# Performance work log

Hardware: AMD Instinct MI355X
Metric: run time of the kernel (lower is better)

## Reference

```python
import jax, jax.numpy as jnp
import numpy as np

B, N, D, F, NRBF, H = 8, 256, 3, 32, 50, 128
EPS = 1e-6

# Levi-Civita tensor [3,3,3]
LC = jnp.array(np.array([[[0, 0, 0], [0, 0, 1], [0, -1, 0]],
                         [[0, 0, -1], [0, 0, 0], [1, 0, 0]],
                         [[0, 1, 0], [-1, 0, 0], [0, 0, 0]]], dtype=np.float32))

# off-diagonal neighbor indices: OFFD[i] = all j != i  -> [N, N-1]
OFFD = np.stack([np.concatenate([np.arange(i), np.arange(i + 1, N)]) for i in range(N)])


def mlp(x, W1, b1, W2, b2):
    return jax.nn.silu(x @ W1 + b1) @ W2 + b2


def rbf_encode(d, mus, gamma):
    # d: [B,N,N-1,1] -> [B,N,N-1,NRBF]
    return jnp.exp(-gamma * (d - mus) ** 2)


def setup_inputs() -> dict:
    key = jax.random.key(0)
    ks = jax.random.split(key, 8)
    p = lambda k, shape: 0.1 * jax.random.normal(k, shape, dtype=jnp.float32)
    IN = NRBF + 2 * F    # 114: rbfs + self feats + 'other' feats
    INF = NRBF + F       # 82: rbfs + softmax feats
    return {
        't': jnp.zeros((1,), jnp.float32),
        'state': jax.random.normal(ks[0], (B, N * D + N * F), dtype=jnp.float32),
        'mus': jnp.linspace(0.0, 5.0, NRBF, dtype=jnp.float32),
        'gamma': jnp.float32(10.0),
        's1_W1': p(ks[1], (IN, H)), 's1_b1': jnp.zeros((H,), jnp.float32),
        's1_W2': p(ks[2], (H, 1)), 's1_b2': jnp.zeros((1,), jnp.float32),
        's2_W1': p(ks[3], (IN, H)), 's2_b1': jnp.zeros((H,), jnp.float32),
        's2_W2': p(ks[4], (H, 1)), 's2_b2': jnp.zeros((1,), jnp.float32),
        'f_W1': p(ks[5], (INF, H)), 'f_b1': jnp.zeros((H,), jnp.float32),
        'f_W2': p(ks[6], (H, F)), 'f_b2': jnp.zeros((F,), jnp.float32),
    }


def reference(t, state, mus, gamma,
              s1_W1, s1_b1, s1_W2, s1_b2,
              s2_W1, s2_b1, s2_W2, s2_b2,
              f_W1, f_b1, f_W2, f_b2):
    x = state[:, :N * D].reshape(B, N, D)
    feats = state[:, N * D:].reshape(B, N, F)

    # distance vectors r[b,i,k] = x[b,i] - x[b, OFFD[i,k]]  -> [B,N,N-1,D]
    r = x[:, :, None, :] - x[:, OFFD, :]
    d = jnp.sqrt(jnp.sum(r ** 2, -1, keepdims=True) + EPS)  # [B,N,N-1,1]

    # NOTE: the torch tile+transpose+diagonal_filter yields other_feats[b,i,k] = feats[b,i]
    # (self features broadcast over neighbors); reproduced faithfully.
    feats_i = jnp.broadcast_to(feats[:, :, None, :], (B, N, N - 1, F))
    other_feats = feats_i

    rbfs = rbf_encode(d, mus, gamma)  # [B,N,N-1,NRBF]
    inp = jnp.concatenate([rbfs, feats_i, other_feats], -1)  # [B,N,N-1,114]

    # exact trace: grad of s1 wrt d contracted with r2d (torch.autograd.grad equivalent)
    def s1_of_d(dd):
        rb = rbf_encode(dd, mus, gamma)
        return mlp(jnp.concatenate([rb, feats_i, other_feats], -1), s1_W1, s1_b1, s1_W2, s1_b2)

    s1, vjp_fn = jax.vjp(s1_of_d, d)  # s1: [B,N,N-1,1]
    r2d = jnp.sum(r ** 2, -1, keepdims=True) / d
    (gd,) = vjp_fn(r2d)
    first_sum = jnp.sum(gd, axis=(1, 2))          # [B,1]
    second_sum = jnp.sum(s1 * D, axis=(1, 2))     # [B,1]
    trace = (first_sum + second_sum) / (N - 1)    # [B,1]

    s2 = mlp(inp, s2_W1, s2_b1, s2_W2, s2_b2)     # [B,N,N-1,1]

    # feature dynamics: cat(rbfs, softmax(other_feats)) -> MLP -> mean over neighbors
    inp_f = jnp.concatenate([rbfs, jax.nn.softmax(other_feats, axis=-1)], -1)
    v_feats = mlp(inp_f, f_W1, f_b1, f_W2, f_b2).mean(axis=2).reshape(B, N * F)

    v_x = (r * s1).mean(axis=2)  # [B,N,D]
    rr = jnp.einsum('ofi,nabf,nai->nabo', LC, r, v_x)  # [B,N,N-1,D]
    v_x = v_x + (rr * s2).mean(axis=2)
    v_x = (v_x - v_x.mean(axis=1, keepdims=True)).reshape(B, N * D)  # remove_mean

    v = jnp.concatenate([v_x, v_feats], axis=-1)  # [B, N*D + N*F]
    return v, trace
```

## Files before the change

kernel.cpp:

```cpp
#include <hip/hip_runtime.h>
#include <math.h>

#define Bn 8
#define Nn 256
#define Fn 32
#define NRBF 50
#define Hn 128
#define NK 255
#define ROW 8960
#define EPSf 1e-6f
#define KP 64
#define L2E 1.44269504f

typedef __attribute__((ext_vector_type(8))) __bf16 b8;
typedef __attribute__((ext_vector_type(4))) float f32x4;

__device__ __forceinline__ float fast_sig(float z) {
    return __builtin_amdgcn_rcpf(1.f + __builtin_amdgcn_exp2f(-z * L2E));
}

__device__ __forceinline__ int aswz(int row, int ch) {
    return row * KP + ((ch ^ (row & 7)) << 3);
}

__global__ __launch_bounds__(256) void prep_kernel(
    const float* __restrict__ s1_W1, const float* __restrict__ s1_b1,
    const float* __restrict__ s2_W1, const float* __restrict__ s2_b1,
    const float* __restrict__ f_W1,  const float* __restrict__ f_b1,
    const float* __restrict__ mus,   const float* __restrict__ state,
    __bf16* __restrict__ Wb,
    float* __restrict__ zb1, float* __restrict__ zb2, float* __restrict__ zb3)
{
    const int tid = threadIdx.x;
    if (blockIdx.x < 128) {
        int idx = blockIdx.x * 256 + tid;
        int g = idx >> 13;
        int h = (idx >> 6) & 127;
        int k = idx & 63;
        float v = 0.f;
        if (k < NRBF) {
            if (g == 0)      v = s1_W1[k * Hn + h];
            else if (g == 1) v = s1_W1[k * Hn + h] * mus[k];
            else if (g == 2) v = s2_W1[k * Hn + h];
            else             v = f_W1[k * Hn + h];
        }
        Wb[idx] = (__bf16)v;
        return;
    }

    const int p = blockIdx.x - 128;
    const int b = p >> 8, i = p & 255;

    __shared__ float ff[Fn], sf[Fn];
    if (tid < Fn) ff[tid] = state[b * ROW + Nn * 3 + i * Fn + tid];
    __syncthreads();
    if (tid < Fn) {
        float mx = -1e30f;
        for (int f = 0; f < Fn; f++) mx = fmaxf(mx, ff[f]);
        sf[tid] = __builtin_amdgcn_exp2f((ff[tid] - mx) * L2E);
    }
    __syncthreads();
    if (tid < Fn) {
        float s = 0.f;
        for (int f = 0; f < Fn; f++) s += sf[f];
        sf[tid] = sf[tid] * __builtin_amdgcn_rcpf(s);
    }
    __syncthreads();

    const int h = tid & 127;
    if (tid < 128) {
        float z1 = s1_b1[h], z2 = s2_b1[h];
        for (int f = 0; f < Fn; f++) {
            float fv = ff[f];
            z1 += fv * (s1_W1[(NRBF + f) * Hn + h] + s1_W1[(NRBF + Fn + f) * Hn + h]);
            z2 += fv * (s2_W1[(NRBF + f) * Hn + h] + s2_W1[(NRBF + Fn + f) * Hn + h]);
        }
        zb1[p * Hn + h] = z1;
        zb2[p * Hn + h] = z2;
    } else {
        float zf = f_b1[h];
        for (int f = 0; f < Fn; f++)
            zf += sf[f] * f_W1[(NRBF + f) * Hn + h];
        zb3[p * Hn + h] = zf;
    }
}

__global__ __launch_bounds__(256, 2) void pair_kernel(
    const float* __restrict__ state,
    const float* __restrict__ mus,   const float* __restrict__ gammap,
    const float* __restrict__ s1_W2, const float* __restrict__ s1_b2,
    const float* __restrict__ s2_W2, const float* __restrict__ s2_b2,
    const float* __restrict__ f_W2,  const float* __restrict__ f_b2,
    const __bf16* __restrict__ Wb,
    const float* __restrict__ zb1, const float* __restrict__ zb2,
    const float* __restrict__ zb3,
    float* __restrict__ vx_pre, float* __restrict__ tr_part,
    float* __restrict__ out)
{
    const int i = blockIdx.x, b = blockIdx.y;
    const int pi = b * Nn + i;
    const int tid  = threadIdx.x;
    const int w    = tid >> 6;
    const int lane = tid & 63;
    const int c    = lane & 15;
    const int q    = lane >> 4;

    __shared__ __attribute__((aligned(16))) __bf16 As[256 * KP];
    __shared__ float xpos[Nn * 3];
    __shared__ float musS[52];
    __shared__ float zf1s[Hn], zf2s[Hn], zffs[Hn];
    __shared__ float sW2a[Hn], sW2b[Hn];
    __shared__ float afsumsh[Hn];
    __shared__ float accum7[8];

    for (int t = tid; t < Nn * 3; t += 256) xpos[t] = state[b * ROW + t];
    if (tid < NRBF) musS[tid] = mus[tid];
    if (tid < Hn) {
        zf1s[tid] = zb1[pi * Hn + tid];
        zf2s[tid] = zb2[pi * Hn + tid];
        zffs[tid] = zb3[pi * Hn + tid];
        sW2a[tid] = s1_W2[tid];
        sW2b[tid] = s2_W2[tid];
        afsumsh[tid] = 0.f;
    }
    if (tid < 8) accum7[tid] = 0.f;
    __syncthreads();

    const float gamma = gammap[0];

    {
        const float valid = (tid < NK) ? 1.f : 0.f;
        const int   kk    = (tid < NK) ? tid : 0;
        const int   j     = kk + (kk >= i ? 1 : 0);
        float rx = (xpos[i * 3 + 0] - xpos[j * 3 + 0]) * valid;
        float ry = (xpos[i * 3 + 1] - xpos[j * 3 + 1]) * valid;
        float rz = (xpos[i * 3 + 2] - xpos[j * 3 + 2]) * valid;
        float ssq = rx * rx + ry * ry + rz * rz;
        float dd  = sqrtf(ssq + EPSf);
        const float ngl = -gamma * L2E;
        #pragma unroll
        for (int ch = 0; ch < 8; ch++) {
            b8 v;
            #pragma unroll
            for (int jj = 0; jj < 8; jj++) {
                int m = ch * 8 + jj;
                float rv = 0.f;
                if (m < NRBF) {
                    float t = dd - musS[m];
                    rv = __builtin_amdgcn_exp2f(ngl * t * t) * valid;
                }
                v[jj] = (__bf16)rv;
            }
            *(b8*)&As[aswz(tid, ch)] = v;
        }
    }
    __syncthreads();

    const int row0 = w * 64;

    float s1p[16], ds1a[16], ds1b[16], s2p[16];
    #pragma unroll
    for (int t = 0; t < 16; t++) { s1p[t] = 0.f; ds1a[t] = 0.f; ds1b[t] = 0.f; s2p[t] = 0.f; }

    {
        b8 a0[4], a1[4];
        #pragma unroll
        for (int mc = 0; mc < 4; mc++) {
            int rrow = row0 + mc * 16 + c;
            a0[mc] = *(const b8*)&As[aswz(rrow, q)];
            a1[mc] = *(const b8*)&As[aswz(rrow, 4 + q)];
        }
        for (int nt = 0; nt < 8; nt++) {
            int h = nt * 16 + c;
            const b8* B0 = (const b8*)&Wb[(0 * Hn + h) * KP];
            const b8* B1 = (const b8*)&Wb[(1 * Hn + h) * KP];
            b8 b00 = B0[q], b01 = B0[4 + q];
            b8 b10 = B1[q], b11 = B1[4 + q];
            float w2  = sW2a[h];
            float zf1 = zf1s[h];
            #pragma unroll
            for (int mc = 0; mc < 4; mc++) {
                f32x4 acc1 = {0.f, 0.f, 0.f, 0.f}, accm = {0.f, 0.f, 0.f, 0.f};
                acc1 = __builtin_amdgcn_mfma_f32_16x16x32_bf16(a0[mc], b00, acc1, 0, 0, 0);
                acc1 = __builtin_amdgcn_mfma_f32_16x16x32_bf16(a1[mc], b01, acc1, 0, 0, 0);
                accm = __builtin_amdgcn_mfma_f32_16x16x32_bf16(a0[mc], b10, accm, 0, 0, 0);
                accm = __builtin_amdgcn_mfma_f32_16x16x32_bf16(a1[mc], b11, accm, 0, 0, 0);
                #pragma unroll
                for (int r = 0; r < 4; r++) {
                    int idx = mc * 4 + r;
                    float zr1 = acc1[r];
                    float z1  = zr1 + zf1;
                    float sig = fast_sig(z1);
                    s1p[idx]  = fmaf(z1 * sig, w2, s1p[idx]);
                    float cc  = w2 * (sig * fmaf(z1, 1.f - sig, 1.f));
                    ds1a[idx] = fmaf(cc, zr1, ds1a[idx]);
                    ds1b[idx] = fmaf(cc, accm[r], ds1b[idx]);
                }
            }
        }
    }

    {
        b8 a0[4], a1[4];
        #pragma unroll
        for (int mc = 0; mc < 4; mc++) {
            int rrow = row0 + mc * 16 + c;
            a0[mc] = *(const b8*)&As[aswz(rrow, q)];
            a1[mc] = *(const b8*)&As[aswz(rrow, 4 + q)];
        }
        for (int nt = 0; nt < 8; nt++) {
            int h = nt * 16 + c;
            const b8* B2 = (const b8*)&Wb[(2 * Hn + h) * KP];
            b8 b20 = B2[q], b21 = B2[4 + q];
            float w2  = sW2b[h];
            float zf2 = zf2s[h];
            #pragma unroll
            for (int mc = 0; mc < 4; mc++) {
                f32x4 acc = {0.f, 0.f, 0.f, 0.f};
                acc = __builtin_amdgcn_mfma_f32_16x16x32_bf16(a0[mc], b20, acc, 0, 0, 0);
                acc = __builtin_amdgcn_mfma_f32_16x16x32_bf16(a1[mc], b21, acc, 0, 0, 0);
                #pragma unroll
                for (int r = 0; r < 4; r++) {
                    int idx = mc * 4 + r;
                    float z2  = acc[r] + zf2;
                    s2p[idx]  = fmaf(z2 * fast_sig(z2), w2, s2p[idx]);
                }
            }
        }
    }

    {
        const float b2_1 = (c == 0) ? s1_b2[0] : 0.f;
        const float b2_2 = (c == 0) ? s2_b2[0] : 0.f;
        const float n2g  = -2.f * gamma;
        const float xi0 = xpos[i * 3 + 0], xi1 = xpos[i * 3 + 1], xi2 = xpos[i * 3 + 2];
        float p0 = 0.f, p1 = 0.f, p2 = 0.f, p3 = 0.f, p4 = 0.f, p5 = 0.f, p6 = 0.f;
        #pragma unroll
        for (int mc = 0; mc < 4; mc++)
            #pragma unroll
            for (int r = 0; r < 4; r++) {
                int idx = mc * 4 + r;
                int row = row0 + mc * 16 + q * 4 + r;
                if (row < NK) {
                    int j = row + (row >= i ? 1 : 0);
                    float rx = xi0 - xpos[j * 3 + 0];
                    float ry = xi1 - xpos[j * 3 + 1];
                    float rz = xi2 - xpos[j * 3 + 2];
                    float ssq = rx * rx + ry * ry + rz * rz;
                    float dd  = sqrtf(ssq + EPSf);
                    float e1  = s1p[idx] + b2_1;
                    float e2  = s2p[idx] + b2_2;
                    float e3  = fmaf(dd, ds1a[idx], -ds1b[idx]);
                    float fr  = n2g * ssq * __builtin_amdgcn_rcpf(dd);
                    p0 = fmaf(rx, e1, p0); p1 = fmaf(ry, e1, p1); p2 = fmaf(rz, e1, p2);
                    p3 = fmaf(rx, e2, p3); p4 = fmaf(ry, e2, p4); p5 = fmaf(rz, e2, p5);
                    p6 = fmaf(fr, e3, fmaf(3.f, e1, p6));
                }
            }
        float ps[7] = {p0, p1, p2, p3, p4, p5, p6};
        #pragma unroll
        for (int off = 1; off < 64; off <<= 1)
            #pragma unroll
            for (int t = 0; t < 7; t++) ps[t] += __shfl_xor(ps[t], off, 64);
        if (lane == 0) {
            #pragma unroll
            for (int t = 0; t < 7; t++) atomicAdd(&accum7[t], ps[t]);
        }
    }

    {
        b8 a0[4], a1[4];
        #pragma unroll
        for (int mc = 0; mc < 4; mc++) {
            int rrow = row0 + mc * 16 + c;
            a0[mc] = *(const b8*)&As[aswz(rrow, q)];
            a1[mc] = *(const b8*)&As[aswz(rrow, 4 + q)];
        }
        for (int nt = 0; nt < 8; nt++) {
            int h = nt * 16 + c;
            const b8* B3 = (const b8*)&Wb[(3 * Hn + h) * KP];
            b8 b30 = B3[q], b31 = B3[4 + q];
            float zff = zffs[h];
            float afp = 0.f;
            #pragma unroll
            for (int mc = 0; mc < 4; mc++) {
                f32x4 acc = {0.f, 0.f, 0.f, 0.f};
                acc = __builtin_amdgcn_mfma_f32_16x16x32_bf16(a0[mc], b30, acc, 0, 0, 0);
                acc = __builtin_amdgcn_mfma_f32_16x16x32_bf16(a1[mc], b31, acc, 0, 0, 0);
                #pragma unroll
                for (int r = 0; r < 4; r++) {
                    int row = row0 + mc * 16 + q * 4 + r;
                    float z  = acc[r] + zff;
                    float av = z * fast_sig(z);
                    afp += (row < NK) ? av : 0.f;
                }
            }
            afp += __shfl_xor(afp, 16, 64);
            afp += __shfl_xor(afp, 32, 64);
            if (lane < 16) atomicAdd(&afsumsh[h], afp);
        }
    }
    __syncthreads();

    if (tid == 0) {
        const float inv = 1.f / 255.f;
        float vx0 = accum7[0] * inv, vx1 = accum7[1] * inv, vx2 = accum7[2] * inv;
        float cx = (accum7[4] * vx2 - accum7[5] * vx1) * inv;
        float cy = (accum7[5] * vx0 - accum7[3] * vx2) * inv;
        float cz = (accum7[3] * vx1 - accum7[4] * vx0) * inv;
        vx_pre[pi * 4 + 0] = vx0 + cx;
        vx_pre[pi * 4 + 1] = vx1 + cy;
        vx_pre[pi * 4 + 2] = vx2 + cz;
        tr_part[pi] = accum7[6];
    }

    if (tid < Fn) {
        float acc = 0.f;
        for (int h = 0; h < Hn; h++) acc = fmaf(afsumsh[h], f_W2[h * Fn + tid], acc);
        out[b * ROW + Nn * 3 + i * Fn + tid] = fmaf(acc, 1.f / 255.f, f_b2[tid]);
    }
}

__global__ __launch_bounds__(256) void finalize_kernel(
    const float* __restrict__ vx_pre, const float* __restrict__ tr_part,
    float* __restrict__ out)
{
    int b = blockIdx.x, tid = threadIdx.x;
    int bi = b * Nn + tid;
    float v0 = vx_pre[bi * 4 + 0];
    float v1 = vx_pre[bi * 4 + 1];
    float v2 = vx_pre[bi * 4 + 2];
    float tr = tr_part[bi];

    __shared__ float red[4][4];
    __shared__ float fin[4];
    float vals[4] = {v0, v1, v2, tr};
    #pragma unroll
    for (int cc = 0; cc < 4; cc++) {
        float v = vals[cc];
        #pragma unroll
        for (int off = 32; off; off >>= 1) v += __shfl_down(v, off, 64);
        if ((tid & 63) == 0) red[tid >> 6][cc] = v;
    }
    __syncthreads();
    if (tid < 4) fin[tid] = red[0][tid] + red[1][tid] + red[2][tid] + red[3][tid];
    __syncthreads();

    out[b * ROW + tid * 3 + 0] = v0 - fin[0] * (1.f / 256.f);
    out[b * ROW + tid * 3 + 1] = v1 - fin[1] * (1.f / 256.f);
    out[b * ROW + tid * 3 + 2] = v2 - fin[2] * (1.f / 256.f);
    if (tid == 0) out[Bn * ROW + b] = fin[3] * (1.f / 255.f);
}

extern "C" void kernel_launch(void* const* d_in, const int* in_sizes, int n_in,
                              void* d_out, int out_size, void* d_ws, size_t ws_size,
                              hipStream_t stream)
{
    const float* state = (const float*)d_in[1];
    const float* mus   = (const float*)d_in[2];
    const float* gam   = (const float*)d_in[3];
    const float* s1_W1 = (const float*)d_in[4];
    const float* s1_b1 = (const float*)d_in[5];
    const float* s1_W2 = (const float*)d_in[6];
    const float* s1_b2 = (const float*)d_in[7];
    const float* s2_W1 = (const float*)d_in[8];
    const float* s2_b1 = (const float*)d_in[9];
    const float* s2_W2 = (const float*)d_in[10];
    const float* s2_b2 = (const float*)d_in[11];
    const float* f_W1  = (const float*)d_in[12];
    const float* f_b1  = (const float*)d_in[13];
    const float* f_W2  = (const float*)d_in[14];
    const float* f_b2  = (const float*)d_in[15];

    char* wsb = (char*)d_ws;
    __bf16* Wb   = (__bf16*)wsb;
    float* zb1   = (float*)(wsb + 65536);
    float* zb2   = zb1 + Bn * Nn * Hn;
    float* zb3   = zb2 + Bn * Nn * Hn;
    float* vx_pre  = zb3 + Bn * Nn * Hn;
    float* tr_part = vx_pre + Bn * Nn * 4;
    float* out   = (float*)d_out;

    prep_kernel<<<128 + Bn * Nn, 256, 0, stream>>>(
        s1_W1, s1_b1, s2_W1, s2_b1, f_W1, f_b1, mus, state, Wb, zb1, zb2, zb3);

    dim3 grid(Nn, Bn);
    pair_kernel<<<grid, 256, 0, stream>>>(state, mus, gam,
        s1_W2, s1_b2, s2_W2, s2_b2, f_W2, f_b2,
        Wb, zb1, zb2, zb3, vx_pre, tr_part, out);

    finalize_kernel<<<Bn, 256, 0, stream>>>(vx_pre, tr_part, out);
}
```

Baseline: 203.0 us.

## Build RBF MFMA operands in registers instead of staging through LDS

New measurement: 207.1 us. 2.0% more time.

```diff
diff --git a/kernel.cpp b/kernel.cpp
--- a/kernel.cpp
+++ b/kernel.cpp
@@ -17,10 +17,6 @@
 
 __device__ __forceinline__ float fast_sig(float z) {
     return __builtin_amdgcn_rcpf(1.f + __builtin_amdgcn_exp2f(-z * L2E));
-}
-
-__device__ __forceinline__ int aswz(int row, int ch) {
-    return row * KP + ((ch ^ (row & 7)) << 3);
 }
 
 __global__ __launch_bounds__(256) void prep_kernel(
@@ -105,7 +101,6 @@
     const int c    = lane & 15;
     const int q    = lane >> 4;
 
-    __shared__ __attribute__((aligned(16))) __bf16 As[256 * KP];
     __shared__ float xpos[Nn * 3];
     __shared__ float musS[52];
     __shared__ float zf1s[Hn], zf2s[Hn], zffs[Hn];
@@ -115,6 +110,7 @@
 
     for (int t = tid; t < Nn * 3; t += 256) xpos[t] = state[b * ROW + t];
     if (tid < NRBF) musS[tid] = mus[tid];
+    if (tid >= NRBF && tid < 52) musS[tid] = 0.f;
     if (tid < Hn) {
         zf1s[tid] = zb1[pi * Hn + tid];
         zf2s[tid] = zb2[pi * Hn + tid];
@@ -127,113 +123,117 @@
     __syncthreads();
 
     const float gamma = gammap[0];
-
-    {
-        const float valid = (tid < NK) ? 1.f : 0.f;
-        const int   kk    = (tid < NK) ? tid : 0;
-        const int   j     = kk + (kk >= i ? 1 : 0);
-        float rx = (xpos[i * 3 + 0] - xpos[j * 3 + 0]) * valid;
-        float ry = (xpos[i * 3 + 1] - xpos[j * 3 + 1]) * valid;
-        float rz = (xpos[i * 3 + 2] - xpos[j * 3 + 2]) * valid;
+    const float ngl   = -gamma * L2E;
+    const int   row0  = w * 64;
+    const float xi0 = xpos[i * 3 + 0], xi1 = xpos[i * 3 + 1], xi2 = xpos[i * 3 + 2];
+
+    b8 a0[4], a1[4];
+    #pragma unroll
+    for (int mc = 0; mc < 4; mc++) {
+        int row = row0 + mc * 16 + c;
+        int kk  = (row < NK) ? row : 0;
+        float valid = (row < NK) ? 1.f : 0.f;
+        int j = kk + (kk >= i ? 1 : 0);
+        float rx = xi0 - xpos[j * 3 + 0];
+        float ry = xi1 - xpos[j * 3 + 1];
+        float rz = xi2 - xpos[j * 3 + 2];
         float ssq = rx * rx + ry * ry + rz * rz;
         float dd  = sqrtf(ssq + EPSf);
-        const float ngl = -gamma * L2E;
-        #pragma unroll
-        for (int ch = 0; ch < 8; ch++) {
-            b8 v;
-            #pragma unroll
-            for (int jj = 0; jj < 8; jj++) {
-                int m = ch * 8 + jj;
-                float rv = 0.f;
-                if (m < NRBF) {
-                    float t = dd - musS[m];
-                    rv = __builtin_amdgcn_exp2f(ngl * t * t) * valid;
-                }
-                v[jj] = (__bf16)rv;
-            }
-            *(b8*)&As[aswz(tid, ch)] = v;
-        }
-    }
-    __syncthreads();
-
-    const int row0 = w * 64;
+        #pragma unroll
+        for (int jj = 0; jj < 8; jj++) {
+            float t = dd - musS[q * 8 + jj];
+            a0[mc][jj] = (__bf16)(__builtin_amdgcn_exp2f(ngl * t * t) * valid);
+        }
+        #pragma unroll
+        for (int jj = 0; jj < 8; jj++) {
+            int k = 32 + q * 8 + jj;
+            float t = dd - musS[(k < NRBF) ? k : 50];
+            float rv = (k < NRBF) ? __builtin_amdgcn_exp2f(ngl * t * t) * valid : 0.f;
+            a1[mc][jj] = (__bf16)rv;
+        }
+    }
 
     float s1p[16], ds1a[16], ds1b[16], s2p[16];
     #pragma unroll
     for (int t = 0; t < 16; t++) { s1p[t] = 0.f; ds1a[t] = 0.f; ds1b[t] = 0.f; s2p[t] = 0.f; }
 
-    {
-        b8 a0[4], a1[4];
+    for (int nt = 0; nt < 8; nt++) {
+        int h = nt * 16 + c;
+        const b8* B0 = (const b8*)&Wb[(0 * Hn + h) * KP];
+        const b8* B1 = (const b8*)&Wb[(1 * Hn + h) * KP];
+        b8 b00 = B0[q], b01 = B0[4 + q];
+        b8 b10 = B1[q], b11 = B1[4 + q];
+        float w2  = sW2a[h];
+        float zf1 = zf1s[h];
         #pragma unroll
         for (int mc = 0; mc < 4; mc++) {
-            int rrow = row0 + mc * 16 + c;
-            a0[mc] = *(const b8*)&As[aswz(rrow, q)];
-            a1[mc] = *(const b8*)&As[aswz(rrow, 4 + q)];
-        }
-        for (int nt = 0; nt < 8; nt++) {
-            int h = nt * 16 + c;
-            const b8* B0 = (const b8*)&Wb[(0 * Hn + h) * KP];
-            const b8* B1 = (const b8*)&Wb[(1 * Hn + h) * KP];
-            b8 b00 = B0[q], b01 = B0[4 + q];
-            b8 b10 = B1[q], b11 = B1[4 + q];
-            float w2  = sW2a[h];
-            float zf1 = zf1s[h];
-            #pragma unroll
-            for (int mc = 0; mc < 4; mc++) {
-                f32x4 acc1 = {0.f, 0.f, 0.f, 0.f}, accm = {0.f, 0.f, 0.f, 0.f};
-                acc1 = __builtin_amdgcn_mfma_f32_16x16x32_bf16(a0[mc], b00, acc1, 0, 0, 0);
-                acc1 = __builtin_amdgcn_mfma_f32_16x16x32_bf16(a1[mc], b01, acc1, 0, 0, 0);
-                accm = __builtin_amdgcn_mfma_f32_16x16x32_bf16(a0[mc], b10, accm, 0, 0, 0);
-                accm = __builtin_amdgcn_mfma_f32_16x16x32_bf16(a1[mc], b11, accm, 0, 0, 0);
-                #pragma unroll
-                for (int r = 0; r < 4; r++) {
-                    int idx = mc * 4 + r;
-                    float zr1 = acc1[r];
-                    float z1  = zr1 + zf1;
-                    float sig = fast_sig(z1);
-                    s1p[idx]  = fmaf(z1 * sig, w2, s1p[idx]);
-                    float cc  = w2 * (sig * fmaf(z1, 1.f - sig, 1.f));
-                    ds1a[idx] = fmaf(cc, zr1, ds1a[idx]);
-                    ds1b[idx] = fmaf(cc, accm[r], ds1b[idx]);
-                }
+            f32x4 acc1 = {0.f, 0.f, 0.f, 0.f}, accm = {0.f, 0.f, 0.f, 0.f};
+            acc1 = __builtin_amdgcn_mfma_f32_16x16x32_bf16(a0[mc], b00, acc1, 0, 0, 0);
+            acc1 = __builtin_amdgcn_mfma_f32_16x16x32_bf16(a1[mc], b01, acc1, 0, 0, 0);
+            accm = __builtin_amdgcn_mfma_f32_16x16x32_bf16(a0[mc], b10, accm, 0, 0, 0);
+            accm = __builtin_amdgcn_mfma_f32_16x16x32_bf16(a1[mc], b11, accm, 0, 0, 0);
+            #pragma unroll
+            for (int r = 0; r < 4; r++) {
+                int idx = mc * 4 + r;
+                float zr1 = acc1[r];
+                float z1  = zr1 + zf1;
+                float sig = fast_sig(z1);
+                s1p[idx]  = fmaf(z1 * sig, w2, s1p[idx]);
+                float cc  = w2 * (sig * fmaf(z1, 1.f - sig, 1.f));
+                ds1a[idx] = fmaf(cc, zr1, ds1a[idx]);
+                ds1b[idx] = fmaf(cc, accm[r], ds1b[idx]);
             }
         }
     }
 
-    {
-        b8 a0[4], a1[4];
+    for (int nt = 0; nt < 8; nt++) {
+        int h = nt * 16 + c;
+        const b8* B2 = (const b8*)&Wb[(2 * Hn + h) * KP];
+        b8 b20 = B2[q], b21 = B2[4 + q];
+        float w2  = sW2b[h];
+        float zf2 = zf2s[h];
         #pragma unroll
         for (int mc = 0; mc < 4; mc++) {
-            int rrow = row0 + mc * 16 + c;
-            a0[mc] = *(const b8*)&As[aswz(rrow, q)];
-            a1[mc] = *(const b8*)&As[aswz(rrow, 4 + q)];
-        }
-        for (int nt = 0; nt < 8; nt++) {
-            int h = nt * 16 + c;
-            const b8* B2 = (const b8*)&Wb[(2 * Hn + h) * KP];
-            b8 b20 = B2[q], b21 = B2[4 + q];
-            float w2  = sW2b[h];
-            float zf2 = zf2s[h];
-            #pragma unroll
-            for (int mc = 0; mc < 4; mc++) {
-                f32x4 acc = {0.f, 0.f, 0.f, 0.f};
-                acc = __builtin_amdgcn_mfma_f32_16x16x32_bf16(a0[mc], b20, acc, 0, 0, 0);
-                acc = __builtin_amdgcn_mfma_f32_16x16x32_bf16(a1[mc], b21, acc, 0, 0, 0);
-                #pragma unroll
-                for (int r = 0; r < 4; r++) {
-                    int idx = mc * 4 + r;
-                    float z2  = acc[r] + zf2;
-                    s2p[idx]  = fmaf(z2 * fast_sig(z2), w2, s2p[idx]);
-                }
+            f32x4 acc = {0.f, 0.f, 0.f, 0.f};
+            acc = __builtin_amdgcn_mfma_f32_16x16x32_bf16(a0[mc], b20, acc, 0, 0, 0);
+            acc = __builtin_amdgcn_mfma_f32_16x16x32_bf16(a1[mc], b21, acc, 0, 0, 0);
+            #pragma unroll
+            for (int r = 0; r < 4; r++) {
+                int idx = mc * 4 + r;
+                float z2  = acc[r] + zf2;
+                s2p[idx]  = fmaf(z2 * fast_sig(z2), w2, s2p[idx]);
             }
         }
+    }
+
+    for (int nt = 0; nt < 8; nt++) {
+        int h = nt * 16 + c;
+        const b8* B3 = (const b8*)&Wb[(3 * Hn + h) * KP];
+        b8 b30 = B3[q], b31 = B3[4 + q];
+        float zff = zffs[h];
+        float afp = 0.f;
+        #pragma unroll
+        for (int mc = 0; mc < 4; mc++) {
+            f32x4 acc = {0.f, 0.f, 0.f, 0.f};
+            acc = __builtin_amdgcn_mfma_f32_16x16x32_bf16(a0[mc], b30, acc, 0, 0, 0);
+            acc = __builtin_amdgcn_mfma_f32_16x16x32_bf16(a1[mc], b31, acc, 0, 0, 0);
+            #pragma unroll
+            for (int r = 0; r < 4; r++) {
+                int row = row0 + mc * 16 + q * 4 + r;
+                float z  = acc[r] + zff;
+                float av = z * fast_sig(z);
+                afp += (row < NK) ? av : 0.f;
+            }
+        }
+        afp += __shfl_xor(afp, 16, 64);
+        afp += __shfl_xor(afp, 32, 64);
+        if (lane < 16) atomicAdd(&afsumsh[h], afp);
     }
 
     {
         const float b2_1 = (c == 0) ? s1_b2[0] : 0.f;
         const float b2_2 = (c == 0) ? s2_b2[0] : 0.f;
         const float n2g  = -2.f * gamma;
-        const float xi0 = xpos[i * 3 + 0], xi1 = xpos[i * 3 + 1], xi2 = xpos[i * 3 + 2];
         float p0 = 0.f, p1 = 0.f, p2 = 0.f, p3 = 0.f, p4 = 0.f, p5 = 0.f, p6 = 0.f;
         #pragma unroll
         for (int mc = 0; mc < 4; mc++)
@@ -247,11 +247,13 @@
                     float ry = xi1 - xpos[j * 3 + 1];
                     float rz = xi2 - xpos[j * 3 + 2];
                     float ssq = rx * rx + ry * ry + rz * rz;
-                    float dd  = sqrtf(ssq + EPSf);
+                    float se  = ssq + EPSf;
+                    float it  = __builtin_amdgcn_rsqf(se);
+                    float dd  = se * it;
                     float e1  = s1p[idx] + b2_1;
                     float e2  = s2p[idx] + b2_2;
                     float e3  = fmaf(dd, ds1a[idx], -ds1b[idx]);
-                    float fr  = n2g * ssq * __builtin_amdgcn_rcpf(dd);
+                    float fr  = n2g * ssq * it;
                     p0 = fmaf(rx, e1, p0); p1 = fmaf(ry, e1, p1); p2 = fmaf(rz, e1, p2);
                     p3 = fmaf(rx, e2, p3); p4 = fmaf(ry, e2, p4); p5 = fmaf(rz, e2, p5);
                     p6 = fmaf(fr, e3, fmaf(3.f, e1, p6));
@@ -265,39 +267,6 @@
         if (lane == 0) {
             #pragma unroll
             for (int t = 0; t < 7; t++) atomicAdd(&accum7[t], ps[t]);
-        }
-    }
-
-    {
-        b8 a0[4], a1[4];
-        #pragma unroll
-        for (int mc = 0; mc < 4; mc++) {
-            int rrow = row0 + mc * 16 + c;
-            a0[mc] = *(const b8*)&As[aswz(rrow, q)];
-            a1[mc] = *(const b8*)&As[aswz(rrow, 4 + q)];
-        }
-        for (int nt = 0; nt < 8; nt++) {
-            int h = nt * 16 + c;
-            const b8* B3 = (const b8*)&Wb[(3 * Hn + h) * KP];
-            b8 b30 = B3[q], b31 = B3[4 + q];
-            float zff = zffs[h];
-            float afp = 0.f;
-            #pragma unroll
-            for (int mc = 0; mc < 4; mc++) {
-                f32x4 acc = {0.f, 0.f, 0.f, 0.f};
-                acc = __builtin_amdgcn_mfma_f32_16x16x32_bf16(a0[mc], b30, acc, 0, 0, 0);
-                acc = __builtin_amdgcn_mfma_f32_16x16x32_bf16(a1[mc], b31, acc, 0, 0, 0);
-                #pragma unroll
-                for (int r = 0; r < 4; r++) {
-                    int row = row0 + mc * 16 + q * 4 + r;
-                    float z  = acc[r] + zff;
-                    float av = z * fast_sig(z);
-                    afp += (row < NK) ? av : 0.f;
-                }
-            }
-            afp += __shfl_xor(afp, 16, 64);
-            afp += __shfl_xor(afp, 32, 64);
-            if (lane < 16) atomicAdd(&afsumsh[h], afp);
         }
     }
     __syncthreads();
```
